# Optimization experiments

Hardware: AMD Instinct MI355X
Metric: run time of the kernel (lower is better)

Reference implementation:

```python
import jax, jax.numpy as jnp
from jax import lax
import numpy as np

B, S, D_IN, D_OUT, LAT, N_STATE = 8, 2048, 1024, 1024, 256, 32
D_INNER, D_CONV, DT_RANK, N_BLK = 2 * D_OUT, 4, D_OUT // 16, 2


def setup_inputs() -> dict:
    key = jax.random.key(0)
    ks = iter(jax.random.split(key, 24))
    r = lambda shp, s=0.02: jax.random.normal(next(ks), shp, dtype=jnp.float32) * s
    inp = {
        "x": jax.random.normal(next(ks), (B, S, D_IN), dtype=jnp.float32),
        "W_in": r((D_IN, D_OUT)), "b_in": jnp.zeros((D_OUT,), jnp.float32),
        "Wa1": r((D_OUT, LAT)), "ba1": jnp.zeros((LAT,), jnp.float32),
        "Wa2": r((LAT, LAT)), "ba2": jnp.zeros((LAT,), jnp.float32),
        # per-block params, leading axis = N_BLK
        "gamma": jnp.ones((N_BLK, D_OUT), jnp.float32),
        "in_proj_w": r((N_BLK, D_OUT, 2 * D_INNER)),
        "conv_w": r((N_BLK, D_INNER, D_CONV), 0.1),
        "conv_b": jnp.zeros((N_BLK, D_INNER), jnp.float32),
        "x_proj_w": r((N_BLK, D_INNER, DT_RANK + 2 * N_STATE)),
        "dt_proj_w": r((N_BLK, DT_RANK, D_INNER), 0.1),
        "dt_proj_b": jnp.full((N_BLK, D_INNER), -4.6, jnp.float32),  # softplus(-4.6)~0.01
        "A_log": jnp.log(jnp.broadcast_to(jnp.arange(1, N_STATE + 1, dtype=jnp.float32), (N_BLK, D_INNER, N_STATE))),
        "D": jnp.ones((N_BLK, D_INNER), jnp.float32),
        "out_proj_w": r((N_BLK, D_INNER, D_OUT)),
    }
    return inp


def rms_norm(x, gamma):
    # F.normalize(x, dim=-1) * sqrt(d) * gamma
    norm = jnp.sqrt(jnp.sum(x * x, axis=-1, keepdims=True))
    return x / jnp.maximum(norm, 1e-12) * (x.shape[-1] ** 0.5) * gamma


def causal_conv1d(x, w, b):
    # x: [b, d, L], w: [d, d_conv] depthwise, causal (left) padding
    y = lax.conv_general_dilated(
        x, w[:, None, :], window_strides=(1,), padding=[(D_CONV - 1, 0)],
        feature_group_count=x.shape[1], dimension_numbers=("NCH", "OIH", "NCH"))
    return y + b[None, :, None]


def selective_scan(dA, dBu, C):
    # dA, dBu: [b, L, d_inner, n], C: [b, L, n] -> y: [b, L, d_inner]
    def step(h, inp):
        dA_t, dBu_t, C_t = inp
        h = dA_t * h + dBu_t
        return h, jnp.einsum("bdn,bn->bd", h, C_t)
    h0 = jnp.zeros(dA.shape[:1] + dA.shape[2:], dA.dtype)
    _, ys = lax.scan(step, h0, (dA.swapaxes(0, 1), dBu.swapaxes(0, 1), C.swapaxes(0, 1)))
    return ys.swapaxes(0, 1)


def mamba(u, in_w, cw, cb, xw, dtw, dtb, A_log, Dp, ow):
    # u: [b, L, d_model]
    xz = u @ in_w                              # [b, L, 2*d_inner]
    xh, z = jnp.split(xz, 2, axis=-1)
    xh = causal_conv1d(xh.swapaxes(1, 2), cw, cb).swapaxes(1, 2)
    xh = jax.nn.silu(xh)                       # [b, L, d_inner]
    xdbc = xh @ xw                             # [b, L, dt_rank + 2n]
    dt, Bm, Cm = jnp.split(xdbc, [DT_RANK, DT_RANK + N_STATE], axis=-1)
    dt = jax.nn.softplus(dt @ dtw + dtb)       # [b, L, d_inner]
    A = -jnp.exp(A_log)                        # [d_inner, n]
    dA = jnp.exp(dt[..., None] * A)            # [b, L, d_inner, n]
    dBu = dt[..., None] * Bm[:, :, None, :] * xh[..., None]
    y = selective_scan(dA, dBu, Cm) + Dp * xh
    y = y * jax.nn.silu(z)
    return y @ ow


def reference(x, W_in, b_in, Wa1, ba1, Wa2, ba2, gamma, in_proj_w, conv_w,
              conv_b, x_proj_w, dt_proj_w, dt_proj_b, A_log, D, out_proj_w):
    out = x @ W_in + b_in                      # [b, s, d]
    length = out.shape[1]
    w = jax.nn.silu(out @ Wa1 + ba1) @ Wa2 + ba2   # [b, s, LAT]
    w1 = jax.nn.softmax(w, axis=-1) * (LAT / length)
    w2 = jax.nn.softmax(w, axis=-2)
    weights = (w1 + w2) * 0.5
    out = jnp.einsum("bsd,bsS->bSd", out, weights)  # [b, LAT, d]
    for i in range(N_BLK):  # residual RMSNorm + Mamba (dropout = identity in eval)
        out = out + mamba(rms_norm(out, gamma[i]), in_proj_w[i], conv_w[i],
                          conv_b[i], x_proj_w[i], dt_proj_w[i], dt_proj_b[i],
                          A_log[i], D[i], out_proj_w[i])
    return out
```

## Files before the change

### kernel.cpp

```cpp
#include <hip/hip_runtime.h>
#include <math.h>
#include <stdint.h>

#define BB 8
#define SS 2048
#define D_IN 1024
#define D_OUTC 1024
#define LATC 256
#define NSTATE 32
#define DINNER 2048
#define DCONV 4
#define DTRANK 64
#define NCH 32

__device__ __forceinline__ float silu_f(float v) { return v * (1.f / (1.f + __expf(-v))); }
__device__ __forceinline__ float softplus_f(float v) {
    return fmaxf(v, 0.f) + log1pf(__expf(-fabsf(v)));
}

typedef short short8 __attribute__((ext_vector_type(8)));
typedef float f32x4 __attribute__((ext_vector_type(4)));

__device__ __forceinline__ unsigned short f2bf(float f) {
    unsigned u = __builtin_bit_cast(unsigned, f);
    u += 0x7FFFu + ((u >> 16) & 1u);
    return (unsigned short)(u >> 16);
}
__device__ __forceinline__ int pack2(float a, float b) {
    return (int)((unsigned)f2bf(a) | ((unsigned)f2bf(b) << 16));
}

typedef const __attribute__((address_space(1))) unsigned int* gas_ptr;
typedef __attribute__((address_space(3))) unsigned int* las_ptr;
__device__ __forceinline__ void gload16(const void* g, void* l) {
    __builtin_amdgcn_global_load_lds(
        reinterpret_cast<gas_ptr>(reinterpret_cast<uintptr_t>(g)),
        reinterpret_cast<las_ptr>(reinterpret_cast<uintptr_t>(l)),
        16, 0, 0);
}

__global__ __launch_bounds__(256) void transp_bf(const float* __restrict__ src,
                                                 unsigned short* __restrict__ dst,
                                                 int K, int N)
{
    __shared__ float tile[32][33];
    const int n0 = blockIdx.x * 32;
    const int k0 = blockIdx.y * 32;
    const int x = threadIdx.x & 31;
    const int y = threadIdx.x >> 5;
#pragma unroll
    for (int j = 0; j < 4; j++)
        tile[y + 8 * j][x] = src[(size_t)(k0 + y + 8 * j) * N + n0 + x];
    __syncthreads();
#pragma unroll
    for (int j = 0; j < 4; j++)
        dst[(size_t)(n0 + y + 8 * j) * K + k0 + x] = f2bf(tile[x][y + 8 * j]);
}

__global__ __launch_bounds__(256) void cvt_bf16(const float* __restrict__ in,
                                                unsigned short* __restrict__ out)
{
    size_t i = ((size_t)blockIdx.x * 256 + threadIdx.x) * 8;
    float4 a = *(const float4*)(in + i);
    float4 b = *(const float4*)(in + i + 4);
    int4 w;
    w.x = pack2(a.x, a.y); w.y = pack2(a.z, a.w);
    w.z = pack2(b.x, b.y); w.w = pack2(b.z, b.w);
    *(int4*)(out + i) = w;
}

__global__ __launch_bounds__(256) void gemm16(
    const unsigned short* __restrict__ A, int lda,
    const unsigned short* __restrict__ BT, int ldb,
    const float* __restrict__ bias,
    float* __restrict__ C, int ldc,
    unsigned short* __restrict__ C16, int ldc16,
    int M, int N, int K, int act, int accum)
{
    __shared__ __align__(16) unsigned short As[2][128 * 32];
    __shared__ __align__(16) unsigned short Bs[2][128 * 32];

    const int tid = threadIdx.x;
    const int lane = tid & 63;
    const int wave = tid >> 6;
    const int wr = wave >> 1;
    const int wc = wave & 1;
    const int quad = lane >> 4;
    const int l16 = lane & 15;

    const int nbx = gridDim.x;
    const int nwg = nbx * gridDim.y;
    const int orig = blockIdx.y * nbx + blockIdx.x;
    const int q = nwg >> 3, r = nwg & 7;
    const int xcd = orig & 7, lid = orig >> 3;
    const int swz = (xcd < r) ? (xcd * (q + 1) + lid)
                              : (r * (q + 1) + (xcd - r) * q + lid);
    const int m0 = (swz / nbx) * 128;
    const int n0 = (swz % nbx) * 128;

    const int srow4 = lane >> 2;
    const int sphys = lane & 3;

    f32x4 acc[4][4];
#pragma unroll
    for (int i = 0; i < 4; i++)
#pragma unroll
        for (int j = 0; j < 4; j++) acc[i][j] = (f32x4){0.f, 0.f, 0.f, 0.f};

    const int nt = K >> 5;

    auto STAGE = [&](int buf, int t) {
        const int k0 = t << 5;
#pragma unroll
        for (int i = 0; i < 2; i++) {
            const int rbase = (wave << 5) + (i << 4);
            const int rr = rbase + srow4;
            const int ls = sphys ^ ((rr >> 1) & 3);
            gload16(A + (size_t)(m0 + rr) * lda + (k0 + (ls << 3)), &As[buf][rbase << 5]);
            gload16(BT + (size_t)(n0 + rr) * ldb + (k0 + (ls << 3)), &Bs[buf][rbase << 5]);
        }
    };

    STAGE(0, 0);
    asm volatile("s_waitcnt vmcnt(0)" ::: "memory");
    __syncthreads();

    int cur = 0;
    for (int t = 0; t < nt; ++t) {
        if (t + 1 < nt) STAGE(cur ^ 1, t + 1);

        short8 af[4], bfr[4];
#pragma unroll
        for (int i = 0; i < 4; i++) {
            const int ar = (wr << 6) + (i << 4) + l16;
            af[i] = *(const short8*)&As[cur][(ar << 5) + ((quad ^ ((ar >> 1) & 3)) << 3)];
            const int br = (wc << 6) + (i << 4) + l16;
            bfr[i] = *(const short8*)&Bs[cur][(br << 5) + ((quad ^ ((br >> 1) & 3)) << 3)];
        }
#pragma unroll
        for (int i = 0; i < 4; i++)
#pragma unroll
            for (int j = 0; j < 4; j++)
                acc[i][j] = __builtin_amdgcn_mfma_f32_16x16x32_bf16(af[i], bfr[j], acc[i][j], 0, 0, 0);

        asm volatile("s_waitcnt vmcnt(0)" ::: "memory");
        __syncthreads();
        cur ^= 1;
    }

#pragma unroll
    for (int j = 0; j < 4; j++) {
        int gn = n0 + wc * 64 + j * 16 + l16;
        float bv = bias ? bias[gn] : 0.f;
#pragma unroll
        for (int i = 0; i < 4; i++) {
#pragma unroll
            for (int r2 = 0; r2 < 4; r2++) {
                int gm = m0 + wr * 64 + i * 16 + quad * 4 + r2;
                float v = acc[i][j][r2] + bv;
                if (act == 1) v = silu_f(v);
                else if (act == 2) v = softplus_f(v);
                if (C) {
                    size_t ci = (size_t)gm * ldc + gn;
                    if (accum) C[ci] += v;
                    else C[ci] = v;
                }
                if (C16) C16[(size_t)gm * ldc16 + gn] = f2bf(v);
            }
        }
    }
}

__global__ __launch_bounds__(256) void gemm_mix(
    const float* __restrict__ A, int lda, long strideA,
    const unsigned short* __restrict__ B16, int ldb, long strideB,
    float* __restrict__ C, int ldc, long strideC,
    int M, int N, int K)
{
    __shared__ __align__(16) unsigned short As[128][40];
    __shared__ __align__(16) unsigned short Bs[128][40];

    const int bz = blockIdx.z;
    const float* Ab = A + (size_t)bz * strideA;
    const unsigned short* Bb = B16 + (size_t)bz * strideB;
    float* Cb = C + (size_t)bz * strideC;

    const int tid = threadIdx.x;
    const int lane = tid & 63;
    const int wave = tid >> 6;
    const int wr = wave >> 1;
    const int wc = wave & 1;
    const int quad = lane >> 4;
    const int l16 = lane & 15;

    const int m0 = blockIdx.y * 128;
    const int n0 = blockIdx.x * 128;

    f32x4 acc[4][4];
#pragma unroll
    for (int i = 0; i < 4; i++)
#pragma unroll
        for (int j = 0; j < 4; j++) acc[i][j] = (f32x4){0.f, 0.f, 0.f, 0.f};

    for (int k0 = 0; k0 < K; k0 += 32) {
        {
            int kr = tid >> 3;
            int x0 = (tid & 7) * 16;
            const float* src = Ab + (size_t)(k0 + kr) * lda + (m0 + x0);
#pragma unroll
            for (int q = 0; q < 4; q++) {
                float4 f = *(const float4*)(src + q * 4);
                As[x0 + q * 4 + 0][kr] = f2bf(f.x);
                As[x0 + q * 4 + 1][kr] = f2bf(f.y);
                As[x0 + q * 4 + 2][kr] = f2bf(f.z);
                As[x0 + q * 4 + 3][kr] = f2bf(f.w);
            }
        }
        {
            int kr = tid >> 3;
            int x0 = (tid & 7) * 16;
            const unsigned short* src = Bb + (size_t)(k0 + kr) * ldb + (n0 + x0);
            short8 v0 = *(const short8*)(src);
            short8 v1 = *(const short8*)(src + 8);
#pragma unroll
            for (int q = 0; q < 8; q++) Bs[x0 + q][kr] = (unsigned short)v0[q];
#pragma unroll
            for (int q = 0; q < 8; q++) Bs[x0 + 8 + q][kr] = (unsigned short)v1[q];
        }
        __syncthreads();

        short8 af[4], bfr[4];
#pragma unroll
        for (int i = 0; i < 4; i++) {
            af[i] = *(const short8*)&As[wr * 64 + i * 16 + l16][quad * 8];
            bfr[i] = *(const short8*)&Bs[wc * 64 + i * 16 + l16][quad * 8];
        }
#pragma unroll
        for (int i = 0; i < 4; i++)
#pragma unroll
            for (int j = 0; j < 4; j++)
                acc[i][j] = __builtin_amdgcn_mfma_f32_16x16x32_bf16(af[i], bfr[j], acc[i][j], 0, 0, 0);
        __syncthreads();
    }

#pragma unroll
    for (int j = 0; j < 4; j++) {
        int gn = n0 + wc * 64 + j * 16 + l16;
#pragma unroll
        for (int i = 0; i < 4; i++) {
#pragma unroll
            for (int r = 0; r < 4; r++) {
                int gm = m0 + wr * 64 + i * 16 + quad * 4 + r;
                Cb[(size_t)gm * ldc + gn] = acc[i][j][r];
            }
        }
    }
}

__global__ __launch_bounds__(256) void gemm_kernel(
    const float* __restrict__ A, int lda, long strideA,
    const float* __restrict__ B, int ldb, long strideB,
    const float* __restrict__ bias,
    float* __restrict__ C, int ldc, long strideC,
    int M, int N, int K, int transA, int act, int accum)
{
    __shared__ float As[16][65];
    __shared__ float Bsh[16][64];

    const int bz = blockIdx.z;
    const float* Ab = A + (size_t)bz * strideA;
    const float* Bb = B + (size_t)bz * strideB;
    float* Cb = C + (size_t)bz * strideC;

    const int tx = threadIdx.x;
    const int ty = threadIdx.y;
    const int tid = ty * 16 + tx;
    const int m0 = blockIdx.y * 64;
    const int n0 = blockIdx.x * 64;

    float acc[4][4];
#pragma unroll
    for (int i = 0; i < 4; i++)
#pragma unroll
        for (int j = 0; j < 4; j++) acc[i][j] = 0.f;

    for (int k0 = 0; k0 < K; k0 += 16) {
        if (!transA) {
            int row = tid >> 2;
            int kc = (tid & 3) * 4;
            int gm = m0 + row;
#pragma unroll
            for (int j = 0; j < 4; j++) {
                int gk = k0 + kc + j;
                As[kc + j][row] = (gm < M && gk < K) ? Ab[(size_t)gm * lda + gk] : 0.f;
            }
        } else {
            int krow = tid >> 4;
            int mc = (tid & 15) * 4;
            int gk = k0 + krow;
#pragma unroll
            for (int j = 0; j < 4; j++) {
                int gm = m0 + mc + j;
                As[krow][mc + j] = (gm < M && gk < K) ? Ab[(size_t)gk * lda + gm] : 0.f;
            }
        }
        {
            int krow = tid >> 4;
            int nc = (tid & 15) * 4;
            int gk = k0 + krow;
#pragma unroll
            for (int j = 0; j < 4; j++) {
                int gn = n0 + nc + j;
                Bsh[krow][nc + j] = (gk < K && gn < N) ? Bb[(size_t)gk * ldb + gn] : 0.f;
            }
        }
        __syncthreads();
#pragma unroll
        for (int k = 0; k < 16; k++) {
            float a[4], bv[4];
#pragma unroll
            for (int i = 0; i < 4; i++) a[i] = As[k][ty * 4 + i];
#pragma unroll
            for (int j = 0; j < 4; j++) bv[j] = Bsh[k][tx * 4 + j];
#pragma unroll
            for (int i = 0; i < 4; i++)
#pragma unroll
                for (int j = 0; j < 4; j++) acc[i][j] += a[i] * bv[j];
        }
        __syncthreads();
    }

#pragma unroll
    for (int i = 0; i < 4; i++) {
        int gm = m0 + ty * 4 + i;
        if (gm >= M) continue;
#pragma unroll
        for (int j = 0; j < 4; j++) {
            int gn = n0 + tx * 4 + j;
            if (gn >= N) continue;
            float v = acc[i][j];
            if (bias) v += bias[gn];
            if (act == 1) v = silu_f(v);
            else if (act == 2) v = softplus_f(v);
            size_t ci = (size_t)gm * ldc + gn;
            if (accum) Cb[ci] += v;
            else Cb[ci] = v;
        }
    }
}

__global__ __launch_bounds__(256) void merge4_kernel(const float* __restrict__ part,
                                                     float* __restrict__ out, int n)
{
    int i = blockIdx.x * 256 + threadIdx.x;
    out[i] = part[i] + part[i + n] + part[i + 2 * n] + part[i + 3 * n];
}

__global__ __launch_bounds__(256) void colstats_part_kernel(const float* __restrict__ w,
                                                            float* __restrict__ part)
{
    int b = blockIdx.x / NCH;
    int ch = blockIdx.x % NCH;
    int l = threadIdx.x;
    const float* base = w + ((size_t)b * SS + (size_t)ch * (SS / NCH)) * LATC + l;
    float m = -1e30f, s = 0.f;
    for (int t = 0; t < SS / NCH; t++) {
        float v = base[(size_t)t * LATC];
        float nm = fmaxf(m, v);
        s = s * __expf(m - nm) + __expf(v - nm);
        m = nm;
    }
    float2* p = (float2*)part;
    p[(size_t)(b * LATC + l) * NCH + ch] = make_float2(m, s);
}

__global__ __launch_bounds__(256) void colstats_merge_kernel(const float* __restrict__ part,
                                                             float* __restrict__ colst)
{
    int idx = blockIdx.x * 256 + threadIdx.x;
    const float2* p = (const float2*)part + (size_t)idx * NCH;
    float m = -1e30f, s = 0.f;
#pragma unroll 4
    for (int c = 0; c < NCH; c++) {
        float2 v = p[c];
        float nm = fmaxf(m, v.x);
        s = s * __expf(m - nm) + v.y * __expf(v.x - nm);
        m = nm;
    }
    colst[idx * 2] = m;
    colst[idx * 2 + 1] = s;
}

__global__ __launch_bounds__(256) void softmix_kernel(float* __restrict__ w,
                                                      const float* __restrict__ colst)
{
    int bs = blockIdx.x;
    int b = bs / SS;
    int l = threadIdx.x;
    float* row = w + (size_t)bs * LATC;
    float v = row[l];

    __shared__ float sm[256];
    sm[l] = v;
    __syncthreads();
    for (int st = 128; st > 0; st >>= 1) {
        if (l < st) sm[l] = fmaxf(sm[l], sm[l + st]);
        __syncthreads();
    }
    float rmax = sm[0];
    __syncthreads();
    float e = __expf(v - rmax);
    sm[l] = e;
    __syncthreads();
    for (int st = 128; st > 0; st >>= 1) {
        if (l < st) sm[l] += sm[l + st];
        __syncthreads();
    }
    float rsum = sm[0];

    float w1 = e / rsum * ((float)LATC / (float)SS);
    float cm = colst[(b * LATC + l) * 2];
    float cs = colst[(b * LATC + l) * 2 + 1];
    float w2 = __expf(v - cm) / cs;
    row[l] = 0.5f * (w1 + w2);
}

__global__ __launch_bounds__(256) void rmsnorm_kernel(const float* __restrict__ x,
                                                      const float* __restrict__ gamma,
                                                      unsigned short* __restrict__ out)
{
    int row = blockIdx.x;
    const float* xr = x + (size_t)row * D_OUTC;
    float v[4];
    float ss = 0.f;
#pragma unroll
    for (int i = 0; i < 4; i++) {
        v[i] = xr[threadIdx.x + i * 256];
        ss += v[i] * v[i];
    }
#pragma unroll
    for (int off = 32; off >= 1; off >>= 1) ss += __shfl_xor(ss, off, 64);
    __shared__ float sred[4];
    int wave = threadIdx.x >> 6;
    if ((threadIdx.x & 63) == 0) sred[wave] = ss;
    __syncthreads();
    float tot = sred[0] + sred[1] + sred[2] + sred[3];
    float inv = 32.0f / fmaxf(sqrtf(tot), 1e-12f);
    unsigned short* outr = out + (size_t)row * D_OUTC;
#pragma unroll
    for (int i = 0; i < 4; i++) {
        int d = threadIdx.x + i * 256;
        outr[d] = f2bf(v[i] * inv * gamma[d]);
    }
}

__global__ __launch_bounds__(256) void conv_silu_kernel(const float* __restrict__ xz,
                                                        const float* __restrict__ cw,
                                                        const float* __restrict__ cb,
                                                        float* __restrict__ xh, int L)
{
    int idx = blockIdx.x * 256 + threadIdx.x;
    int c = idx % DINNER;
    int bl = idx / DINNER;
    int l = bl % L;
    int b = bl / L;
    float acc = cb[c];
#pragma unroll
    for (int j = 0; j < DCONV; j++) {
        int ls = l - (DCONV - 1) + j;
        if (ls >= 0)
            acc += xz[((size_t)(b * L + ls)) * (2 * DINNER) + c] * cw[c * DCONV + j];
    }
    xh[idx] = silu_f(acc);
}

#define SCH 4
__global__ __launch_bounds__(256) void scan_kernel(const float* __restrict__ dty,
                                                   const float* __restrict__ xh,
                                                   const float* __restrict__ xz,
                                                   const float* __restrict__ xdbc,
                                                   const float* __restrict__ A_log,
                                                   const float* __restrict__ Dp,
                                                   unsigned short* __restrict__ ybf,
                                                   int L)
{
    const int t = threadIdx.x;
    const int g = t & 7;
    const int dloc = t >> 3;
    const int b = blockIdx.x >> 6;
    const int d = ((blockIdx.x & 63) << 5) + dloc;

    float4 Av = *(const float4*)(A_log + (size_t)d * NSTATE + g * 4);
    const float A0 = -__expf(Av.x), A1 = -__expf(Av.y), A2 = -__expf(Av.z), A3 = -__expf(Av.w);
    float h0 = 0.f, h1 = 0.f, h2 = 0.f, h3 = 0.f;
    const float Dd = Dp[d];

    const float* pdt = dty + (size_t)b * L * DINNER + d;
    const float* pxh = xh + (size_t)b * L * DINNER + d;
    const float* pz  = xz + (size_t)b * L * 2 * DINNER + DINNER + d;
    const float* pbc = xdbc + (size_t)b * L * 128 + DTRANK + g * 4;
    unsigned short* pout = ybf + (size_t)b * L * DINNER + d;

    float a_dt[SCH], a_x[SCH], a_z[SCH];
    float4 a_B[SCH], a_C[SCH];
    float n_dt[SCH], n_x[SCH], n_z[SCH];
    float4 n_B[SCH], n_C[SCH];

#pragma unroll
    for (int j = 0; j < SCH; j++) {
        a_dt[j] = pdt[(size_t)j * DINNER];
        a_x[j]  = pxh[(size_t)j * DINNER];
        a_z[j]  = pz[(size_t)j * 2 * DINNER];
        a_B[j]  = *(const float4*)(pbc + (size_t)j * 128);
        a_C[j]  = *(const float4*)(pbc + (size_t)j * 128 + NSTATE);
    }

    for (int l0 = 0; l0 < L; l0 += SCH) {
        const int lb = (l0 + SCH < L) ? (l0 + SCH) : l0;
#pragma unroll
        for (int j = 0; j < SCH; j++) {
            n_dt[j] = pdt[(size_t)(lb + j) * DINNER];
            n_x[j]  = pxh[(size_t)(lb + j) * DINNER];
            n_z[j]  = pz[(size_t)(lb + j) * 2 * DINNER];
            n_B[j]  = *(const float4*)(pbc + (size_t)(lb + j) * 128);
            n_C[j]  = *(const float4*)(pbc + (size_t)(lb + j) * 128 + NSTATE);
        }
#pragma unroll
        for (int j = 0; j < SCH; j++) {
            float dtv = a_dt[j], xv = a_x[j], zv = a_z[j];
            float dtx = dtv * xv;
            float e0 = __expf(dtv * A0);
            float e1 = __expf(dtv * A1);
            float e2 = __expf(dtv * A2);
            float e3 = __expf(dtv * A3);
            h0 = e0 * h0 + dtx * a_B[j].x;
            h1 = e1 * h1 + dtx * a_B[j].y;
            h2 = e2 * h2 + dtx * a_B[j].z;
            h3 = e3 * h3 + dtx * a_B[j].w;
            float accv = h0 * a_C[j].x + h1 * a_C[j].y + h2 * a_C[j].z + h3 * a_C[j].w;
            accv += __shfl_xor(accv, 1, 64);
            accv += __shfl_xor(accv, 2, 64);
            accv += __shfl_xor(accv, 4, 64);
            if (g == 0) {
                float yv = (accv + Dd * xv) * silu_f(zv);
                pout[(size_t)(l0 + j) * DINNER] = f2bf(yv);
            }
        }
#pragma unroll
        for (int j = 0; j < SCH; j++) {
            a_dt[j] = n_dt[j]; a_x[j] = n_x[j]; a_z[j] = n_z[j];
            a_B[j] = n_B[j];   a_C[j] = n_C[j];
        }
    }
}


extern "C" void kernel_launch(void* const* d_in, const int* in_sizes, int n_in,
                              void* d_out, int out_size, void* d_ws, size_t ws_size,
                              hipStream_t stream)
{
    const float* x      = (const float*)d_in[0];
    const float* W_in   = (const float*)d_in[1];
    const float* b_in   = (const float*)d_in[2];
    const float* Wa1    = (const float*)d_in[3];
    const float* ba1    = (const float*)d_in[4];
    const float* Wa2    = (const float*)d_in[5];
    const float* ba2    = (const float*)d_in[6];
    const float* gamma  = (const float*)d_in[7];
    const float* in_w   = (const float*)d_in[8];
    const float* conv_w = (const float*)d_in[9];
    const float* conv_b = (const float*)d_in[10];
    const float* x_w    = (const float*)d_in[11];
    const float* dt_w   = (const float*)d_in[12];
    const float* dt_b   = (const float*)d_in[13];
    const float* A_log  = (const float*)d_in[14];
    const float* Dp     = (const float*)d_in[15];
    const float* out_w  = (const float*)d_in[16];
    float* latout = (float*)d_out;

    char* wsb = (char*)d_ws;
    const size_t MB = 1 << 20;

    unsigned short* out0_bf = (unsigned short*)(wsb);
    unsigned short* xbf     = (unsigned short*)(wsb + 32 * MB);
    float*          wbuf    = (float*)(wsb + 64 * MB);
    unsigned short* t1_bf   = (unsigned short*)(wsb + 80 * MB);
    unsigned short* WinT    = (unsigned short*)(wsb + 88 * MB);
    unsigned short* Wa1T    = (unsigned short*)(wsb + 90 * MB);
    unsigned short* Wa2T    = (unsigned short*)(wsb + 90 * MB + 512 * 1024);
    float*          cs_part = (float*)(wsb + 91 * MB);
    float*          colst   = (float*)(wsb + 95 * MB);

    unsigned short* unorm_bf  = (unsigned short*)(wsb);
    float*          xdbc_part = (float*)(wsb + 4 * MB);
    float*          dtbuf     = (float*)(wsb + 8 * MB);
    unsigned short* ybf       = (unsigned short*)(wsb + 24 * MB);
    float*          xz        = (float*)(wsb + 32 * MB);
    float*          xh        = (float*)(wsb + 64 * MB);
    unsigned short* wprojT    = (unsigned short*)(wsb + 80 * MB);
    unsigned short* oprojT    = (unsigned short*)(wsb + 88 * MB);
    float*          xdbc      = (float*)(wsb + 92 * MB);

    dim3 blk(16, 16);
    const int L = LATC;
    const int M1 = BB * SS;
    const int ML = BB * L;

    cvt_bf16<<<dim3((size_t)M1 * D_IN / 2048), dim3(256), 0, stream>>>(x, xbf);
    transp_bf<<<dim3(D_OUTC / 32, D_IN / 32), dim3(256), 0, stream>>>(W_in, WinT, D_IN, D_OUTC);
    transp_bf<<<dim3(LATC / 32, D_OUTC / 32), dim3(256), 0, stream>>>(Wa1, Wa1T, D_OUTC, LATC);
    transp_bf<<<dim3(LATC / 32, LATC / 32), dim3(256), 0, stream>>>(Wa2, Wa2T, LATC, LATC);

    gemm16<<<dim3(D_OUTC / 128, M1 / 128), dim3(256), 0, stream>>>(
        xbf, D_IN, WinT, D_IN, b_in, (float*)nullptr, 0, out0_bf, D_OUTC,
        M1, D_OUTC, D_IN, 0, 0);

    gemm16<<<dim3(LATC / 128, M1 / 128), dim3(256), 0, stream>>>(
        out0_bf, D_OUTC, Wa1T, D_OUTC, ba1, (float*)nullptr, 0, t1_bf, LATC,
        M1, LATC, D_OUTC, 1, 0);

    gemm16<<<dim3(LATC / 128, M1 / 128), dim3(256), 0, stream>>>(
        t1_bf, LATC, Wa2T, LATC, ba2, wbuf, LATC, (unsigned short*)nullptr, 0,
        M1, LATC, LATC, 0, 0);

    colstats_part_kernel<<<dim3(BB * NCH), dim3(256), 0, stream>>>(wbuf, cs_part);
    colstats_merge_kernel<<<dim3(BB * LATC / 256), dim3(256), 0, stream>>>(cs_part, colst);
    softmix_kernel<<<dim3(BB * SS), dim3(256), 0, stream>>>(wbuf, colst);

    gemm_mix<<<dim3(D_OUTC / 128, LATC / 128, BB), dim3(256), 0, stream>>>(
        wbuf, LATC, (long)SS * LATC, out0_bf, D_OUTC, (long)SS * D_OUTC,
        latout, D_OUTC, (long)LATC * D_OUTC, LATC, D_OUTC, SS);

    for (int i = 0; i < 2; i++) {
        const float* in_wi = in_w + (size_t)i * D_OUTC * 2 * DINNER;
        const float* cwi = conv_w + (size_t)i * DINNER * DCONV;
        const float* cbi = conv_b + (size_t)i * DINNER;
        const float* xwi = x_w + (size_t)i * DINNER * (DTRANK + 2 * NSTATE);
        const float* dtwi = dt_w + (size_t)i * DTRANK * DINNER;
        const float* dtbi = dt_b + (size_t)i * DINNER;
        const float* Ali = A_log + (size_t)i * DINNER * NSTATE;
        const float* Dpi = Dp + (size_t)i * DINNER;
        const float* owi = out_w + (size_t)i * DINNER * D_OUTC;
        const float* gi = gamma + (size_t)i * D_OUTC;

        transp_bf<<<dim3(2 * DINNER / 32, D_OUTC / 32), dim3(256), 0, stream>>>(
            in_wi, wprojT, D_OUTC, 2 * DINNER);
        transp_bf<<<dim3(D_OUTC / 32, DINNER / 32), dim3(256), 0, stream>>>(
            owi, oprojT, DINNER, D_OUTC);

        rmsnorm_kernel<<<dim3(ML), dim3(256), 0, stream>>>(latout, gi, unorm_bf);

        gemm16<<<dim3(2 * DINNER / 128, ML / 128), dim3(256), 0, stream>>>(
            unorm_bf, D_OUTC, wprojT, D_OUTC, (const float*)nullptr,
            xz, 2 * DINNER, (unsigned short*)nullptr, 0,
            ML, 2 * DINNER, D_OUTC, 0, 0);

        conv_silu_kernel<<<dim3(BB * L * DINNER / 256), dim3(256), 0, stream>>>(xz, cwi, cbi, xh, L);

        gemm_kernel<<<dim3(128 / 64, ML / 64, 4), blk, 0, stream>>>(
            xh, DINNER, 512, xwi, 128, (long)512 * 128, (const float*)nullptr,
            xdbc_part, 128, (long)ML * 128, ML, 128, 512, 0, 0, 0);
        merge4_kernel<<<dim3(ML * 128 / 256), dim3(256), 0, stream>>>(
            xdbc_part, xdbc, ML * 128);

        gemm_kernel<<<dim3(DINNER / 64, ML / 64, 1), blk, 0, stream>>>(
            xdbc, 128, 0, dtwi, DINNER, 0, dtbi, dtbuf, DINNER, 0, ML, DINNER, DTRANK, 0, 2, 0);

        scan_kernel<<<dim3(BB * DINNER * 8 / 256), dim3(256), 0, stream>>>(
            dtbuf, xh, xz, xdbc, Ali, Dpi, ybf, L);

        gemm16<<<dim3(D_OUTC / 128, ML / 128), dim3(256), 0, stream>>>(
            ybf, DINNER, oprojT, DINNER, (const float*)nullptr,
            latout, D_OUTC, (unsigned short*)nullptr, 0,
            ML, D_OUTC, DINNER, 0, 1);
    }
}
```

Baseline: 1.033 ms.

## Replace gemm_mix with transposes plus batched split-K gemm16

```diff
diff --git a/kernel.cpp b/kernel.cpp
--- a/kernel.cpp
+++ b/kernel.cpp
@@ -41,9 +41,11 @@
 
 __global__ __launch_bounds__(256) void transp_bf(const float* __restrict__ src,
                                                  unsigned short* __restrict__ dst,
-                                                 int K, int N)
+                                                 int K, int N, long zsrc, long zdst)
 {
     __shared__ float tile[32][33];
+    src += (size_t)blockIdx.z * zsrc;
+    dst += (size_t)blockIdx.z * zdst;
     const int n0 = blockIdx.x * 32;
     const int k0 = blockIdx.y * 32;
     const int x = threadIdx.x & 31;
@@ -55,6 +57,26 @@
 #pragma unroll
     for (int j = 0; j < 4; j++)
         dst[(size_t)(n0 + y + 8 * j) * K + k0 + x] = f2bf(tile[x][y + 8 * j]);
+}
+
+__global__ __launch_bounds__(256) void transp16(const unsigned short* __restrict__ src,
+                                                unsigned short* __restrict__ dst,
+                                                int K, int N, long zsrc, long zdst)
+{
+    __shared__ unsigned short tile[32][33];
+    src += (size_t)blockIdx.z * zsrc;
+    dst += (size_t)blockIdx.z * zdst;
+    const int n0 = blockIdx.x * 32;
+    const int k0 = blockIdx.y * 32;
+    const int x = threadIdx.x & 31;
+    const int y = threadIdx.x >> 5;
+#pragma unroll
+    for (int j = 0; j < 4; j++)
+        tile[y + 8 * j][x] = src[(size_t)(k0 + y + 8 * j) * N + n0 + x];
+    __syncthreads();
+#pragma unroll
+    for (int j = 0; j < 4; j++)
+        dst[(size_t)(n0 + y + 8 * j) * K + k0 + x] = tile[x][y + 8 * j];
 }
 
 __global__ __launch_bounds__(256) void cvt_bf16(const float* __restrict__ in,
@@ -75,10 +97,17 @@
     const float* __restrict__ bias,
     float* __restrict__ C, int ldc,
     unsigned short* __restrict__ C16, int ldc16,
-    int M, int N, int K, int act, int accum)
+    int M, int N, int K, int act, int accum,
+    int kspl, long zA, long zB, long zC, long zK)
 {
     __shared__ __align__(16) unsigned short As[2][128 * 32];
     __shared__ __align__(16) unsigned short Bs[2][128 * 32];
+
+    const int bz = blockIdx.z / kspl;
+    const int ks = blockIdx.z % kspl;
+    A += (size_t)bz * zA + (size_t)ks * (size_t)K;
+    BT += (size_t)bz * zB + (size_t)ks * (size_t)K;
+    if (C) C += (size_t)bz * zC + (size_t)ks * zK;
 
     const int tid = threadIdx.x;
     const int lane = tid & 63;
@@ -171,92 +200,6 @@
     }
 }
 
-__global__ __launch_bounds__(256) void gemm_mix(
-    const float* __restrict__ A, int lda, long strideA,
-    const unsigned short* __restrict__ B16, int ldb, long strideB,
-    float* __restrict__ C, int ldc, long strideC,
-    int M, int N, int K)
-{
-    __shared__ __align__(16) unsigned short As[128][40];
-    __shared__ __align__(16) unsigned short Bs[128][40];
-
-    const int bz = blockIdx.z;
-    const float* Ab = A + (size_t)bz * strideA;
-    const unsigned short* Bb = B16 + (size_t)bz * strideB;
-    float* Cb = C + (size_t)bz * strideC;
-
-    const int tid = threadIdx.x;
-    const int lane = tid & 63;
-    const int wave = tid >> 6;
-    const int wr = wave >> 1;
-    const int wc = wave & 1;
-    const int quad = lane >> 4;
-    const int l16 = lane & 15;
-
-    const int m0 = blockIdx.y * 128;
-    const int n0 = blockIdx.x * 128;
-
-    f32x4 acc[4][4];
-#pragma unroll
-    for (int i = 0; i < 4; i++)
-#pragma unroll
-        for (int j = 0; j < 4; j++) acc[i][j] = (f32x4){0.f, 0.f, 0.f, 0.f};
-
-    for (int k0 = 0; k0 < K; k0 += 32) {
-        {
-            int kr = tid >> 3;
-            int x0 = (tid & 7) * 16;
-            const float* src = Ab + (size_t)(k0 + kr) * lda + (m0 + x0);
-#pragma unroll
-            for (int q = 0; q < 4; q++) {
-                float4 f = *(const float4*)(src + q * 4);
-                As[x0 + q * 4 + 0][kr] = f2bf(f.x);
-                As[x0 + q * 4 + 1][kr] = f2bf(f.y);
-                As[x0 + q * 4 + 2][kr] = f2bf(f.z);
-                As[x0 + q * 4 + 3][kr] = f2bf(f.w);
-            }
-        }
-        {
-            int kr = tid >> 3;
-            int x0 = (tid & 7) * 16;
-            const unsigned short* src = Bb + (size_t)(k0 + kr) * ldb + (n0 + x0);
-            short8 v0 = *(const short8*)(src);
-            short8 v1 = *(const short8*)(src + 8);
-#pragma unroll
-            for (int q = 0; q < 8; q++) Bs[x0 + q][kr] = (unsigned short)v0[q];
-#pragma unroll
-            for (int q = 0; q < 8; q++) Bs[x0 + 8 + q][kr] = (unsigned short)v1[q];
-        }
-        __syncthreads();
-
-        short8 af[4], bfr[4];
-#pragma unroll
-        for (int i = 0; i < 4; i++) {
-            af[i] = *(const short8*)&As[wr * 64 + i * 16 + l16][quad * 8];
-            bfr[i] = *(const short8*)&Bs[wc * 64 + i * 16 + l16][quad * 8];
-        }
-#pragma unroll
-        for (int i = 0; i < 4; i++)
-#pragma unroll
-            for (int j = 0; j < 4; j++)
-                acc[i][j] = __builtin_amdgcn_mfma_f32_16x16x32_bf16(af[i], bfr[j], acc[i][j], 0, 0, 0);
-        __syncthreads();
-    }
-
-#pragma unroll
-    for (int j = 0; j < 4; j++) {
-        int gn = n0 + wc * 64 + j * 16 + l16;
-#pragma unroll
-        for (int i = 0; i < 4; i++) {
-#pragma unroll
-            for (int r = 0; r < 4; r++) {
-                int gm = m0 + wr * 64 + i * 16 + quad * 4 + r;
-                Cb[(size_t)gm * ldc + gn] = acc[i][j][r];
-            }
-        }
-    }
-}
-
 __global__ __launch_bounds__(256) void gemm_kernel(
     const float* __restrict__ A, int lda, long strideA,
     const float* __restrict__ B, int ldb, long strideB,
@@ -354,6 +297,13 @@
 {
     int i = blockIdx.x * 256 + threadIdx.x;
     out[i] = part[i] + part[i + n] + part[i + 2 * n] + part[i + 3 * n];
+}
+
+__global__ __launch_bounds__(256) void merge2_kernel(const float* __restrict__ part,
+                                                     float* __restrict__ out, int n)
+{
+    int i = blockIdx.x * 256 + threadIdx.x;
+    out[i] = part[i] + part[i + n];
 }
 
 __global__ __launch_bounds__(256) void colstats_part_kernel(const float* __restrict__ w,
@@ -591,6 +541,10 @@
     float*          cs_part = (float*)(wsb + 91 * MB);
     float*          colst   = (float*)(wsb + 95 * MB);
 
+    unsigned short* out0T   = (unsigned short*)(wsb + 32 * MB);
+    unsigned short* wT      = (unsigned short*)(wsb + 80 * MB);
+    float*          part6   = (float*)(wsb + 64 * MB);
+
     unsigned short* unorm_bf  = (unsigned short*)(wsb);
     float*          xdbc_part = (float*)(wsb + 4 * MB);
     float*          dtbuf     = (float*)(wsb + 8 * MB);
@@ -607,29 +561,38 @@
     const int ML = BB * L;
 
     cvt_bf16<<<dim3((size_t)M1 * D_IN / 2048), dim3(256), 0, stream>>>(x, xbf);
-    transp_bf<<<dim3(D_OUTC / 32, D_IN / 32), dim3(256), 0, stream>>>(W_in, WinT, D_IN, D_OUTC);
-    transp_bf<<<dim3(LATC / 32, D_OUTC / 32), dim3(256), 0, stream>>>(Wa1, Wa1T, D_OUTC, LATC);
-    transp_bf<<<dim3(LATC / 32, LATC / 32), dim3(256), 0, stream>>>(Wa2, Wa2T, LATC, LATC);
+    transp_bf<<<dim3(D_OUTC / 32, D_IN / 32), dim3(256), 0, stream>>>(W_in, WinT, D_IN, D_OUTC, 0, 0);
+    transp_bf<<<dim3(LATC / 32, D_OUTC / 32), dim3(256), 0, stream>>>(Wa1, Wa1T, D_OUTC, LATC, 0, 0);
+    transp_bf<<<dim3(LATC / 32, LATC / 32), dim3(256), 0, stream>>>(Wa2, Wa2T, LATC, LATC, 0, 0);
 
     gemm16<<<dim3(D_OUTC / 128, M1 / 128), dim3(256), 0, stream>>>(
         xbf, D_IN, WinT, D_IN, b_in, (float*)nullptr, 0, out0_bf, D_OUTC,
-        M1, D_OUTC, D_IN, 0, 0);
+        M1, D_OUTC, D_IN, 0, 0, 1, 0, 0, 0, 0);
 
     gemm16<<<dim3(LATC / 128, M1 / 128), dim3(256), 0, stream>>>(
         out0_bf, D_OUTC, Wa1T, D_OUTC, ba1, (float*)nullptr, 0, t1_bf, LATC,
-        M1, LATC, D_OUTC, 1, 0);
+        M1, LATC, D_OUTC, 1, 0, 1, 0, 0, 0, 0);
 
     gemm16<<<dim3(LATC / 128, M1 / 128), dim3(256), 0, stream>>>(
         t1_bf, LATC, Wa2T, LATC, ba2, wbuf, LATC, (unsigned short*)nullptr, 0,
-        M1, LATC, LATC, 0, 0);
+        M1, LATC, LATC, 0, 0, 1, 0, 0, 0, 0);
 
     colstats_part_kernel<<<dim3(BB * NCH), dim3(256), 0, stream>>>(wbuf, cs_part);
     colstats_merge_kernel<<<dim3(BB * LATC / 256), dim3(256), 0, stream>>>(cs_part, colst);
     softmix_kernel<<<dim3(BB * SS), dim3(256), 0, stream>>>(wbuf, colst);
 
-    gemm_mix<<<dim3(D_OUTC / 128, LATC / 128, BB), dim3(256), 0, stream>>>(
-        wbuf, LATC, (long)SS * LATC, out0_bf, D_OUTC, (long)SS * D_OUTC,
-        latout, D_OUTC, (long)LATC * D_OUTC, LATC, D_OUTC, SS);
+    transp16<<<dim3(D_OUTC / 32, SS / 32, BB), dim3(256), 0, stream>>>(
+        out0_bf, out0T, SS, D_OUTC, (long)SS * D_OUTC, (long)D_OUTC * SS);
+    transp_bf<<<dim3(LATC / 32, SS / 32, BB), dim3(256), 0, stream>>>(
+        wbuf, wT, SS, LATC, (long)SS * LATC, (long)LATC * SS);
+    gemm16<<<dim3(D_OUTC / 128, LATC / 128, BB * 2), dim3(256), 0, stream>>>(
+        wT, SS, out0T, SS, (const float*)nullptr,
+        part6, D_OUTC, (unsigned short*)nullptr, 0,
+        LATC, D_OUTC, SS / 2, 0, 0,
+        2, (long)LATC * SS, (long)D_OUTC * SS, (long)LATC * D_OUTC,
+        (long)BB * LATC * D_OUTC);
+    merge2_kernel<<<dim3(BB * LATC * D_OUTC / 256), dim3(256), 0, stream>>>(
+        part6, latout, BB * LATC * D_OUTC);
 
     for (int i = 0; i < 2; i++) {
         const float* in_wi = in_w + (size_t)i * D_OUTC * 2 * DINNER;
@@ -644,16 +607,16 @@
         const float* gi = gamma + (size_t)i * D_OUTC;
 
         transp_bf<<<dim3(2 * DINNER / 32, D_OUTC / 32), dim3(256), 0, stream>>>(
-            in_wi, wprojT, D_OUTC, 2 * DINNER);
+            in_wi, wprojT, D_OUTC, 2 * DINNER, 0, 0);
         transp_bf<<<dim3(D_OUTC / 32, DINNER / 32), dim3(256), 0, stream>>>(
-            owi, oprojT, DINNER, D_OUTC);
+            owi, oprojT, DINNER, D_OUTC, 0, 0);
 
         rmsnorm_kernel<<<dim3(ML), dim3(256), 0, stream>>>(latout, gi, unorm_bf);
 
         gemm16<<<dim3(2 * DINNER / 128, ML / 128), dim3(256), 0, stream>>>(
             unorm_bf, D_OUTC, wprojT, D_OUTC, (const float*)nullptr,
             xz, 2 * DINNER, (unsigned short*)nullptr, 0,
-            ML, 2 * DINNER, D_OUTC, 0, 0);
+            ML, 2 * DINNER, D_OUTC, 0, 0, 1, 0, 0, 0, 0);
 
         conv_silu_kernel<<<dim3(BB * L * DINNER / 256), dim3(256), 0, stream>>>(xz, cwi, cbi, xh, L);
 
@@ -672,6 +635,6 @@
         gemm16<<<dim3(D_OUTC / 128, ML / 128), dim3(256), 0, stream>>>(
             ybf, DINNER, oprojT, DINNER, (const float*)nullptr,
             latout, D_OUTC, (unsigned short*)nullptr, 0,
-            ML, D_OUTC, DINNER, 0, 1);
-    }
-}
+            ML, D_OUTC, DINNER, 0, 1, 1, 0, 0, 0, 0);
+    }
+}
```

After: 995.7 us. -3.6%, faster.
